# Optimization experiments

Measured on AMD Instinct MI355X. Metric: run time of the kernel, lower is better.

The kernel has to match this reference:

```python
import jax, jax.numpy as jnp
import numpy as np

IN_FEATURES = 8192
OUT_FEATURES = 8192
BATCH_TOKENS = 64
QMAX = 255  # uint8-style storage range


def setup_inputs() -> dict:
    key = jax.random.key(0)
    k_x, k_w, k_s, k_z, k_b = jax.random.split(key, 5)
    x = jax.random.normal(k_x, (BATCH_TOKENS, IN_FEATURES), dtype=jnp.float32)
    # quantized weight stored as integer codes in [0, 255], per-output-channel qparams
    qweight = jax.random.randint(k_w, (OUT_FEATURES, IN_FEATURES), 0, QMAX + 1, dtype=jnp.int32)
    scales = jax.random.uniform(k_s, (OUT_FEATURES,), dtype=jnp.float32, minval=0.001, maxval=0.02)
    zero_points = jax.random.randint(k_z, (OUT_FEATURES,), 100, 156, dtype=jnp.int32)
    bias = jax.random.normal(k_b, (OUT_FEATURES,), dtype=jnp.float32)
    return {"x": x, "qweight": qweight, "scales": scales, "zero_points": zero_points, "bias": bias}


def reference(x, qweight, scales, zero_points, bias):
    # Dequantize per-output-channel affine quantized weight: W = (q - zp) * scale
    # qweight: [out, in], scales/zero_points: [out]
    w = (qweight.astype(jnp.float32) - zero_points.astype(jnp.float32)[:, None]) * scales[:, None]
    # y = x @ W^T + b : [tokens, out]
    return jnp.einsum('ti,oi->to', x, w) + bias
```

## Files before the change

kernel.cpp:

```cpp
#include <hip/hip_runtime.h>

#define T_DIM 64
#define K_DIM 8192
#define N_DIM 8192
#define KSPLIT 8
#define KC (K_DIM / KSPLIT)
#define BN 128
#define NBX (N_DIM / BN)
#define BK 64
#define NT (KC / BK)

typedef __fp16 half8_t __attribute__((ext_vector_type(8)));
typedef __fp16 half2_t __attribute__((ext_vector_type(2)));
typedef float  f32x4   __attribute__((ext_vector_type(4)));
typedef int    i32x4   __attribute__((ext_vector_type(4)));

__global__ __launch_bounds__(256) void prep_kernel(const float* __restrict__ x,
                                                   __fp16* __restrict__ xh,
                                                   float* __restrict__ rowsum_part) {
    const int t = blockIdx.x >> 2;
    const int q = blockIdx.x & 3;
    const int kbase = q * (K_DIM / 4) + threadIdx.x * 8;
    const float* xr = x + (size_t)t * K_DIM + kbase;
    __fp16* xhr = xh + (size_t)t * K_DIM + kbase;

    f32x4 v0 = *(const f32x4*)xr;
    f32x4 v1 = *(const f32x4*)(xr + 4);
    half8_t h;
    h[0] = (__fp16)v0[0]; h[1] = (__fp16)v0[1]; h[2] = (__fp16)v0[2]; h[3] = (__fp16)v0[3];
    h[4] = (__fp16)v1[0]; h[5] = (__fp16)v1[1]; h[6] = (__fp16)v1[2]; h[7] = (__fp16)v1[3];
    *(half8_t*)xhr = h;

    float s = 0.0f;
    #pragma unroll
    for (int i = 0; i < 8; ++i) s += (float)h[i];

    #pragma unroll
    for (int off = 32; off > 0; off >>= 1) s += __shfl_down(s, off, 64);
    __shared__ float red[4];
    const int lane = threadIdx.x & 63;
    const int w = threadIdx.x >> 6;
    if (lane == 0) red[w] = s;
    __syncthreads();
    if (threadIdx.x == 0) rowsum_part[t * 4 + q] = red[0] + red[1] + red[2] + red[3];
}

__global__ __launch_bounds__(256, 2) void woq_gemm_kernel(
        const int* __restrict__ qw, const __fp16* __restrict__ xh,
        float* __restrict__ part) {
    __shared__ int ldsB[2][128 * BK];

    const int bx = blockIdx.x;
    const int bz = blockIdx.y;
    const int tid = threadIdx.x;
    const int wid = __builtin_amdgcn_readfirstlane(tid >> 6);
    const int lane = tid & 63;
    const int r = lane & 15;
    const int g = lane >> 4;

    const int n_base = bx * BN;
    const int k0 = bz * KC;

    const __fp16* aptr = xh + (size_t)r * K_DIM + k0 + g * 8;

    f32x4 acc[4][2] = {};

#define STAGE(buf, kt) do {                                                       \
        _Pragma("unroll")                                                         \
        for (int j = 0; j < 8; ++j) {                                             \
            const int row_t = wid * 32 + j * 4 + g;                               \
            const int* src = qw + (size_t)(n_base + row_t) * K_DIM + k0           \
                             + (kt) * BK + ((r ^ (row_t & 15)) << 2);             \
            int* dst = &ldsB[buf][(wid * 32 + j * 4) * BK];                       \
            __builtin_amdgcn_global_load_lds(                                     \
                (const __attribute__((address_space(1))) void*)src,               \
                (__attribute__((address_space(3))) void*)dst, 16, 0, 0);          \
        }                                                                         \
    } while (0)

#define COMPUTE(buf, kt) do {                                                     \
        _Pragma("unroll")                                                         \
        for (int s = 0; s < 2; ++s) {                                             \
            half8_t af[4];                                                        \
            _Pragma("unroll")                                                     \
            for (int m = 0; m < 4; ++m)                                           \
                af[m] = *(const half8_t*)(aptr + (size_t)m * 16 * K_DIM           \
                                          + (kt) * BK + s * 32);                  \
            half8_t bf[2];                                                        \
            _Pragma("unroll")                                                     \
            for (int n = 0; n < 2; ++n) {                                         \
                const int row_t = wid * 32 + n * 16 + r;                          \
                i32x4 q0 = *(const i32x4*)&ldsB[buf][row_t * BK                   \
                                + (((s * 8 + g * 2 + 0) ^ r) << 2)];              \
                i32x4 q1 = *(const i32x4*)&ldsB[buf][row_t * BK                   \
                                + (((s * 8 + g * 2 + 1) ^ r) << 2)];              \
                union { half8_t h8; half2_t h2[4]; } u;                           \
                u.h2[0] = __builtin_amdgcn_cvt_pkrtz((float)q0[0], (float)q0[1]); \
                u.h2[1] = __builtin_amdgcn_cvt_pkrtz((float)q0[2], (float)q0[3]); \
                u.h2[2] = __builtin_amdgcn_cvt_pkrtz((float)q1[0], (float)q1[1]); \
                u.h2[3] = __builtin_amdgcn_cvt_pkrtz((float)q1[2], (float)q1[3]); \
                bf[n] = u.h8;                                                     \
            }                                                                     \
            _Pragma("unroll")                                                     \
            for (int m = 0; m < 4; ++m)                                           \
                _Pragma("unroll")                                                 \
                for (int n = 0; n < 2; ++n)                                       \
                    acc[m][n] = __builtin_amdgcn_mfma_f32_16x16x32_f16(           \
                        af[m], bf[n], acc[m][n], 0, 0, 0);                        \
        }                                                                         \
    } while (0)

    STAGE(0, 0);
    __syncthreads();

    for (int kt = 0; kt < NT; kt += 2) {
        if (kt + 1 < NT) STAGE(1, kt + 1);
        COMPUTE(0, kt);
        __syncthreads();
        if (kt + 2 < NT) STAGE(0, kt + 2);
        COMPUTE(1, kt + 1);
        __syncthreads();
    }

    float* pp = part + (((size_t)bz * NBX + bx) * 4 + wid) * 2048 + g * 16 + r;
    #pragma unroll
    for (int n = 0; n < 2; ++n)
        #pragma unroll
        for (int m = 0; m < 4; ++m)
            #pragma unroll
            for (int j = 0; j < 4; ++j)
                pp[((n * 4 + m) * 4 + j) * 64] = acc[m][n][j];
}

__global__ __launch_bounds__(256) void reduce_kernel(
        const float* __restrict__ part, const float* __restrict__ rowsum_part,
        const float* __restrict__ scales, const int* __restrict__ zps,
        const float* __restrict__ bias, float* __restrict__ out) {
    const int idx = blockIdx.x * 256 + threadIdx.x;
    const int e = idx * 4;
    const int t = e >> 13;
    const int c = e & (N_DIM - 1);
    const int bx = c >> 7;
    const int wid = (c >> 5) & 3;
    const int n = (c >> 4) & 1;
    const int r0 = c & 15;
    const int m = t >> 4;
    const int g = (t >> 2) & 3;
    const int j = t & 3;

    const size_t off = ((size_t)bx * 4 + wid) * 2048 + ((n * 4 + m) * 4 + j) * 64 + g * 16 + r0;
    f32x4 s = {0.f, 0.f, 0.f, 0.f};
    #pragma unroll
    for (int bz = 0; bz < KSPLIT; ++bz)
        s += *(const f32x4*)(part + (size_t)bz * (NBX * 4 * 2048) + off);

    const float rs = rowsum_part[t * 4 + 0] + rowsum_part[t * 4 + 1] +
                     rowsum_part[t * 4 + 2] + rowsum_part[t * 4 + 3];

    f32x4 sc = *(const f32x4*)(scales + c);
    i32x4 zp = *(const i32x4*)(zps + c);
    f32x4 bv = *(const f32x4*)(bias + c);
    f32x4 y;
    #pragma unroll
    for (int i = 0; i < 4; ++i)
        y[i] = sc[i] * (s[i] - (float)zp[i] * rs) + bv[i];
    *(f32x4*)(out + e) = y;
}

extern "C" void kernel_launch(void* const* d_in, const int* in_sizes, int n_in,
                              void* d_out, int out_size, void* d_ws, size_t ws_size,
                              hipStream_t stream) {
    const float* x      = (const float*)d_in[0];
    const int*   qw     = (const int*)d_in[1];
    const float* scales = (const float*)d_in[2];
    const int*   zps    = (const int*)d_in[3];
    const float* bias   = (const float*)d_in[4];
    float* out = (float*)d_out;

    __fp16* xh          = (__fp16*)d_ws;
    float*  rowsum_part = (float*)((char*)d_ws + (1u << 20));
    float*  part        = (float*)((char*)d_ws + (2u << 20));

    prep_kernel<<<256, 256, 0, stream>>>(x, xh, rowsum_part);
    woq_gemm_kernel<<<dim3(NBX, KSPLIT), 256, 0, stream>>>(qw, xh, part);
    reduce_kernel<<<(T_DIM * N_DIM / 4) / 256, 256, 0, stream>>>(
        part, rowsum_part, scales, zps, bias, out);
}
```

Before: 426.0 us.

## Drop split-K and fuse epilogue into GEMM with narrow N tiles

Removes the K-split and the separate reduce kernel. Each 512-thread block now owns 32 output columns over the full K, with 8 waves tiling 4 token groups by 2 column groups, and applies the scale, zero-point and bias epilogue directly. This avoids the partial-sum write and read traffic and one kernel launch. In exchange each block runs a long serial K loop with a single accumulator per wave. The x fragments are now reloaded from global memory by every block, with 256 blocks in flight.

Result: faster. 383.3 us (-10.0%).

```diff
diff --git a/kernel.cpp b/kernel.cpp
--- a/kernel.cpp
+++ b/kernel.cpp
@@ -3,12 +3,10 @@
 #define T_DIM 64
 #define K_DIM 8192
 #define N_DIM 8192
-#define KSPLIT 8
-#define KC (K_DIM / KSPLIT)
-#define BN 128
-#define NBX (N_DIM / BN)
-#define BK 64
-#define NT (KC / BK)
+#define BN 32
+#define BK 256
+#define NT (K_DIM / BK)
+#define NBLK (N_DIM / BN)
 
 typedef __fp16 half8_t __attribute__((ext_vector_type(8)));
 typedef __fp16 half2_t __attribute__((ext_vector_type(2)));
@@ -45,33 +43,36 @@
     if (threadIdx.x == 0) rowsum_part[t * 4 + q] = red[0] + red[1] + red[2] + red[3];
 }
 
-__global__ __launch_bounds__(256, 2) void woq_gemm_kernel(
+__global__ __launch_bounds__(512, 1) void woq_gemm_kernel(
         const int* __restrict__ qw, const __fp16* __restrict__ xh,
-        float* __restrict__ part) {
-    __shared__ int ldsB[2][128 * BK];
+        const float* __restrict__ rowsum_part, const float* __restrict__ scales,
+        const int* __restrict__ zps, const float* __restrict__ bias,
+        float* __restrict__ out) {
+    __shared__ int ldsB[2][BN * BK];
 
     const int bx = blockIdx.x;
-    const int bz = blockIdx.y;
+    const int cbase = bx * BN;
     const int tid = threadIdx.x;
-    const int wid = __builtin_amdgcn_readfirstlane(tid >> 6);
+    const int w = __builtin_amdgcn_readfirstlane(tid >> 6);
     const int lane = tid & 63;
     const int r = lane & 15;
     const int g = lane >> 4;
+    const int wn = w >> 2;
+    const int wm = w & 3;
 
-    const int n_base = bx * BN;
-    const int k0 = bz * KC;
+    const __fp16* aptr = xh + (size_t)(wm * 16 + r) * K_DIM + g * 8;
+    const int ldsrow = wn * 16 + r;
+    const int sw = ldsrow & 7;
 
-    const __fp16* aptr = xh + (size_t)r * K_DIM + k0 + g * 8;
-
-    f32x4 acc[4][2] = {};
+    f32x4 acc = {0.f, 0.f, 0.f, 0.f};
 
 #define STAGE(buf, kt) do {                                                       \
         _Pragma("unroll")                                                         \
-        for (int j = 0; j < 8; ++j) {                                             \
-            const int row_t = wid * 32 + j * 4 + g;                               \
-            const int* src = qw + (size_t)(n_base + row_t) * K_DIM + k0           \
-                             + (kt) * BK + ((r ^ (row_t & 15)) << 2);             \
-            int* dst = &ldsB[buf][(wid * 32 + j * 4) * BK];                       \
+        for (int i = 0; i < 4; ++i) {                                             \
+            const int row = w * 4 + i;                                            \
+            const int* src = qw + (size_t)(cbase + row) * K_DIM + (kt) * BK       \
+                             + ((lane ^ (row & 7)) << 2);                         \
+            int* dst = &ldsB[buf][row * BK];                                      \
             __builtin_amdgcn_global_load_lds(                                     \
                 (const __attribute__((address_space(1))) void*)src,               \
                 (__attribute__((address_space(3))) void*)dst, 16, 0, 0);          \
@@ -80,91 +81,39 @@
 
 #define COMPUTE(buf, kt) do {                                                     \
         _Pragma("unroll")                                                         \
-        for (int s = 0; s < 2; ++s) {                                             \
-            half8_t af[4];                                                        \
-            _Pragma("unroll")                                                     \
-            for (int m = 0; m < 4; ++m)                                           \
-                af[m] = *(const half8_t*)(aptr + (size_t)m * 16 * K_DIM           \
-                                          + (kt) * BK + s * 32);                  \
-            half8_t bf[2];                                                        \
-            _Pragma("unroll")                                                     \
-            for (int n = 0; n < 2; ++n) {                                         \
-                const int row_t = wid * 32 + n * 16 + r;                          \
-                i32x4 q0 = *(const i32x4*)&ldsB[buf][row_t * BK                   \
-                                + (((s * 8 + g * 2 + 0) ^ r) << 2)];              \
-                i32x4 q1 = *(const i32x4*)&ldsB[buf][row_t * BK                   \
-                                + (((s * 8 + g * 2 + 1) ^ r) << 2)];              \
-                union { half8_t h8; half2_t h2[4]; } u;                           \
-                u.h2[0] = __builtin_amdgcn_cvt_pkrtz((float)q0[0], (float)q0[1]); \
-                u.h2[1] = __builtin_amdgcn_cvt_pkrtz((float)q0[2], (float)q0[3]); \
-                u.h2[2] = __builtin_amdgcn_cvt_pkrtz((float)q1[0], (float)q1[1]); \
-                u.h2[3] = __builtin_amdgcn_cvt_pkrtz((float)q1[2], (float)q1[3]); \
-                bf[n] = u.h8;                                                     \
-            }                                                                     \
-            _Pragma("unroll")                                                     \
-            for (int m = 0; m < 4; ++m)                                           \
-                _Pragma("unroll")                                                 \
-                for (int n = 0; n < 2; ++n)                                       \
-                    acc[m][n] = __builtin_amdgcn_mfma_f32_16x16x32_f16(           \
-                        af[m], bf[n], acc[m][n], 0, 0, 0);                        \
+        for (int ks = 0; ks < BK / 32; ++ks) {                                    \
+            half8_t af = *(const half8_t*)(aptr + (size_t)(kt) * BK + ks * 32);   \
+            const int c0 = ks * 8 + g * 2;                                        \
+            i32x4 q0 = *(const i32x4*)&ldsB[buf][ldsrow * BK + (((c0)^sw) << 2)]; \
+            i32x4 q1 = *(const i32x4*)&ldsB[buf][ldsrow * BK + (((c0+1)^sw)<<2)]; \
+            union { half8_t h8; half2_t h2[4]; } u;                               \
+            u.h2[0] = __builtin_amdgcn_cvt_pkrtz((float)q0[0], (float)q0[1]);     \
+            u.h2[1] = __builtin_amdgcn_cvt_pkrtz((float)q0[2], (float)q0[3]);     \
+            u.h2[2] = __builtin_amdgcn_cvt_pkrtz((float)q1[0], (float)q1[1]);     \
+            u.h2[3] = __builtin_amdgcn_cvt_pkrtz((float)q1[2], (float)q1[3]);     \
+            acc = __builtin_amdgcn_mfma_f32_16x16x32_f16(af, u.h8, acc, 0, 0, 0); \
         }                                                                         \
     } while (0)
 
     STAGE(0, 0);
     __syncthreads();
-
-    for (int kt = 0; kt < NT; kt += 2) {
-        if (kt + 1 < NT) STAGE(1, kt + 1);
-        COMPUTE(0, kt);
-        __syncthreads();
-        if (kt + 2 < NT) STAGE(0, kt + 2);
-        COMPUTE(1, kt + 1);
+    for (int kt = 0; kt < NT; ++kt) {
+        if (kt + 1 < NT) STAGE((kt + 1) & 1, kt + 1);
+        COMPUTE(kt & 1, kt);
         __syncthreads();
     }
 
-    float* pp = part + (((size_t)bz * NBX + bx) * 4 + wid) * 2048 + g * 16 + r;
+    const int c = cbase + wn * 16 + r;
+    const float sc = scales[c];
+    const float zp = (float)zps[c];
+    const float bv = bias[c];
     #pragma unroll
-    for (int n = 0; n < 2; ++n)
-        #pragma unroll
-        for (int m = 0; m < 4; ++m)
-            #pragma unroll
-            for (int j = 0; j < 4; ++j)
-                pp[((n * 4 + m) * 4 + j) * 64] = acc[m][n][j];
-}
-
-__global__ __launch_bounds__(256) void reduce_kernel(
-        const float* __restrict__ part, const float* __restrict__ rowsum_part,
-        const float* __restrict__ scales, const int* __restrict__ zps,
-        const float* __restrict__ bias, float* __restrict__ out) {
-    const int idx = blockIdx.x * 256 + threadIdx.x;
-    const int e = idx * 4;
-    const int t = e >> 13;
-    const int c = e & (N_DIM - 1);
-    const int bx = c >> 7;
-    const int wid = (c >> 5) & 3;
-    const int n = (c >> 4) & 1;
-    const int r0 = c & 15;
-    const int m = t >> 4;
-    const int g = (t >> 2) & 3;
-    const int j = t & 3;
-
-    const size_t off = ((size_t)bx * 4 + wid) * 2048 + ((n * 4 + m) * 4 + j) * 64 + g * 16 + r0;
-    f32x4 s = {0.f, 0.f, 0.f, 0.f};
-    #pragma unroll
-    for (int bz = 0; bz < KSPLIT; ++bz)
-        s += *(const f32x4*)(part + (size_t)bz * (NBX * 4 * 2048) + off);
-
-    const float rs = rowsum_part[t * 4 + 0] + rowsum_part[t * 4 + 1] +
-                     rowsum_part[t * 4 + 2] + rowsum_part[t * 4 + 3];
-
-    f32x4 sc = *(const f32x4*)(scales + c);
-    i32x4 zp = *(const i32x4*)(zps + c);
-    f32x4 bv = *(const f32x4*)(bias + c);
-    f32x4 y;
-    #pragma unroll
-    for (int i = 0; i < 4; ++i)
-        y[i] = sc[i] * (s[i] - (float)zp[i] * rs) + bv[i];
-    *(f32x4*)(out + e) = y;
+    for (int j = 0; j < 4; ++j) {
+        const int t = wm * 16 + g * 4 + j;
+        const float rs = rowsum_part[t * 4 + 0] + rowsum_part[t * 4 + 1] +
+                         rowsum_part[t * 4 + 2] + rowsum_part[t * 4 + 3];
+        out[(size_t)t * N_DIM + c] = sc * (acc[j] - zp * rs) + bv;
+    }
 }
 
 extern "C" void kernel_launch(void* const* d_in, const int* in_sizes, int n_in,
@@ -179,10 +128,8 @@
 
     __fp16* xh          = (__fp16*)d_ws;
     float*  rowsum_part = (float*)((char*)d_ws + (1u << 20));
-    float*  part        = (float*)((char*)d_ws + (2u << 20));
 
     prep_kernel<<<256, 256, 0, stream>>>(x, xh, rowsum_part);
-    woq_gemm_kernel<<<dim3(NBX, KSPLIT), 256, 0, stream>>>(qw, xh, part);
-    reduce_kernel<<<(T_DIM * N_DIM / 4) / 256, 256, 0, stream>>>(
-        part, rowsum_part, scales, zps, bias, out);
+    woq_gemm_kernel<<<NBLK, 512, 0, stream>>>(qw, xh, rowsum_part,
+                                              scales, zps, bias, out);
 }
```
